# Kernel tuning notes

Hardware: AMD Instinct MI355X
Metric: run time of the kernel (lower is better)

The kernel has to match this reference:

```python
import jax, jax.numpy as jnp
import numpy as np

BN_EPS = 1e-5
B, L, D = 16, 2048, 1024
OS = 64          # attnList[0]
NC = 256         # candidates per sample
CLASS_NUM = 8921
LAB = 1024


def setup_inputs() -> dict:
    key = jax.random.key(0)
    ks = jax.random.split(key, 8)
    scale_a = 1.0 / np.sqrt(D)
    return {
        "X": jax.random.normal(ks[0], (B, L, D), jnp.float32),
        "candidate": jax.random.randint(ks[1], (B, NC), 0, CLASS_NUM, jnp.int64),
        "a_w": jax.random.normal(ks[2], (D, OS), jnp.float32) * scale_a,
        "a_b": jnp.zeros((OS,), jnp.float32),
        "h_w": jax.random.normal(ks[3], (D, LAB), jnp.float32) * scale_a,
        "h_b": jnp.zeros((LAB,), jnp.float32),
        "bn_gamma": jax.random.uniform(ks[4], (LAB,), jnp.float32, 0.5, 1.5),
        "bn_beta": jax.random.normal(ks[5], (LAB,), jnp.float32) * 0.1,
        "bn_mean": jnp.zeros((LAB,), jnp.float32),
        "bn_var": jnp.ones((LAB,), jnp.float32),
        "labDescVec": jax.random.normal(ks[6], (CLASS_NUM, LAB), jnp.float32),
    }


def reference(X, candidate, a_w, a_b, h_w, h_b, bn_gamma, bn_beta, bn_mean, bn_var, labDescVec):
    # --- attention-pooling layer (attnList has one entry) ---
    # alpha: softmax over the sequence dim (dim=1 in torch)
    alpha = jax.nn.softmax(jnp.einsum('bld,do->blo', X, a_w) + a_b, axis=1)  # [B,L,OS]
    Xp = jnp.einsum('blo,bld->bod', alpha, X)                                # [B,OS,D]
    Xp = jnp.einsum('bod,dh->boh', Xp, h_w) + h_b                            # [B,OS,LAB]
    # BatchNorm1d over feature dim (eval mode: running stats)
    Xp = (Xp - bn_mean) * (bn_gamma / jnp.sqrt(bn_var + BN_EPS)) + bn_beta
    Xp = jax.nn.relu(Xp)  # dropout is identity at inference
    # --- candidate attention ---
    batchLabelVec = labDescVec[candidate]                                    # [B,NC,LAB]
    scores = jnp.einsum('boh,bch->boc', Xp, batchLabelVec)                   # [B,OS,NC]
    alpha2 = jax.nn.softmax(scores, axis=1)                                  # softmax over OS (dim=1)
    out = jnp.einsum('boc,boh->bch', alpha2, Xp)                             # [B,NC,LAB]
    return out
```

## Files before the change

kernel.cpp:

```cpp
#include <hip/hip_runtime.h>
#include <hip/hip_bf16.h>
#include <math.h>

#define Bb   16
#define Ll   2048
#define Dd   1024
#define OSo  64
#define NCc  256
#define LABh 1024
#define BN_EPS 1e-5f

typedef short s8v  __attribute__((ext_vector_type(8)));
typedef short s4v  __attribute__((ext_vector_type(4)));
typedef float f32x4 __attribute__((ext_vector_type(4)));

__device__ __forceinline__ short f2b(float f) {
    __hip_bfloat16 h = __float2bfloat16(f);
    short s;
    __builtin_memcpy(&s, &h, 2);
    return s;
}
__device__ __forceinline__ float b2f(short s) {
    union { unsigned u; float f; } v; v.u = ((unsigned)(unsigned short)s) << 16;
    return v.f;
}
__device__ __forceinline__ void g2lds16(const void* g, void* l) {
    __builtin_amdgcn_global_load_lds(
        (const __attribute__((address_space(1))) void*)g,
        (__attribute__((address_space(3))) void*)l, 16, 0, 0);
}
__device__ __forceinline__ void fastbar() {
    asm volatile("s_waitcnt lgkmcnt(0)\n\ts_barrier" ::: "memory");
}
__device__ __forceinline__ int swi(int row, int kElem) {
    return (row * 128 + ((kElem * 2) ^ ((row & 7) << 4))) >> 1;
}
__device__ __forceinline__ f32x4 MF(s8v a, s8v b, f32x4 c) {
    return __builtin_amdgcn_mfma_f32_16x16x32_bf16(a, b, c, 0, 0, 0);
}

__global__ __launch_bounds__(256) void k0(const float* __restrict__ h_w,
                                          const float* __restrict__ a_w,
                                          short* __restrict__ h_wT,
                                          short* __restrict__ a_wT) {
    __shared__ float t[64][68];
    const int tid = threadIdx.x, id = blockIdx.x;
    const float* src; short* dst; int srw, d0, y0;
    if (id < 256) { src = h_w; dst = h_wT; srw = LABh; d0 = (id & 15) * 64; y0 = (id >> 4) * 64; }
    else          { src = a_w; dst = a_wT; srw = OSo;  d0 = (id - 256) * 64; y0 = 0; }
    const int r = tid >> 2, cofs = (tid & 3) * 16;
    #pragma unroll
    for (int w = 0; w < 4; ++w) {
        float4 v = *(const float4*)&src[(size_t)(d0 + r) * srw + y0 + cofs + w * 4];
        t[r][cofs + w * 4 + 0] = v.x;
        t[r][cofs + w * 4 + 1] = v.y;
        t[r][cofs + w * 4 + 2] = v.z;
        t[r][cofs + w * 4 + 3] = v.w;
    }
    __syncthreads();
    s8v o0, o1;
    #pragma unroll
    for (int e = 0; e < 8; ++e) { o0[e] = f2b(t[cofs + e][r]); o1[e] = f2b(t[cofs + 8 + e][r]); }
    *(s8v*)&dst[(size_t)(y0 + r) * Dd + d0 + cofs]     = o0;
    *(s8v*)&dst[(size_t)(y0 + r) * Dd + d0 + cofs + 8] = o1;
}

__global__ __launch_bounds__(256) void k1(const float* __restrict__ X,
                                          const short* __restrict__ a_wT,
                                          float* __restrict__ St) {
    __shared__ __align__(16) char smem[49152];
    float (*ts)[65] = (float(*)[65])smem;
    const int tid = threadIdx.x, lane = tid & 63, wave = tid >> 6;
    const int wm = wave >> 1, wn = wave & 1;
    const int b = blockIdx.y, l0 = blockIdx.x * 64;
    const float* Xb = X + ((size_t)b * Ll + l0) * Dd;
    const int akb = (lane & 15) * 16;
    const int bkb = (lane & 7) * 16;
    f32x4 acc[2][2] = {};

    auto issue = [&](int t, int k0) {
        char* Ab = smem + (t & 1) * 16384;
        #pragma unroll
        for (int q = 0; q < 4; ++q) {
            const int chunk = wave * 4 + q;
            const int row = chunk * 4 + (lane >> 4);
            const char* g = (const char*)Xb + (size_t)row * 4096 + k0 * 4
                          + (akb ^ ((row & 7) << 4));
            g2lds16(g, Ab + chunk * 1024);
        }
        char* Bbuf = smem + 32768 + (t & 1) * 8192;
        #pragma unroll
        for (int q = 0; q < 2; ++q) {
            const int chunk = wave * 2 + q;
            const int row = chunk * 8 + (lane >> 3);
            const char* g = (const char*)a_wT + (size_t)row * 2048 + k0 * 2
                          + (bkb ^ ((row & 7) << 4));
            g2lds16(g, Bbuf + chunk * 1024);
        }
    };

    issue(0, 0);
    #pragma unroll
    for (int t = 0; t < 16; ++t) {
        if (t < 15) issue(t + 1, (t + 1) * 64);
        __syncthreads();
        const char* Ab = smem + (t & 1) * 16384;
        const char* Bbuf = smem + 32768 + (t & 1) * 8192;
        #pragma unroll
        for (int kk = 0; kk < 2; ++kk) {
            s8v a[2], bv[2];
            #pragma unroll
            for (int i = 0; i < 2; ++i) {
                const int row = wm * 32 + i * 16 + (lane & 15);
                const int sw = (row & 7) << 4;
                const int kbyte = kk * 128 + (lane >> 4) * 32;
                float4 v0 = *(const float4*)(Ab + row * 256 + ((kbyte) ^ sw));
                float4 v1 = *(const float4*)(Ab + row * 256 + ((kbyte + 16) ^ sw));
                s8v s;
                s[0]=f2b(v0.x); s[1]=f2b(v0.y); s[2]=f2b(v0.z); s[3]=f2b(v0.w);
                s[4]=f2b(v1.x); s[5]=f2b(v1.y); s[6]=f2b(v1.z); s[7]=f2b(v1.w);
                a[i] = s;
            }
            #pragma unroll
            for (int j = 0; j < 2; ++j) {
                const int row = wn * 32 + j * 16 + (lane & 15);
                const int sw = (row & 7) << 4;
                const int kbyte = kk * 64 + (lane >> 4) * 16;
                bv[j] = *(const s8v*)(Bbuf + row * 128 + (kbyte ^ sw));
            }
            #pragma unroll
            for (int i = 0; i < 2; ++i)
                #pragma unroll
                for (int j = 0; j < 2; ++j)
                    acc[i][j] = MF(a[i], bv[j], acc[i][j]);
        }
        __syncthreads();
    }
    #pragma unroll
    for (int i = 0; i < 2; ++i)
        #pragma unroll
        for (int j = 0; j < 2; ++j)
            #pragma unroll
            for (int rr = 0; rr < 4; ++rr)
                ts[wm * 32 + i * 16 + (lane >> 4) * 4 + rr][wn * 32 + j * 16 + (lane & 15)] = acc[i][j][rr];
    __syncthreads();
    const int o = tid >> 2, lofs = (tid & 3) * 16;
    float* Sp = St + ((size_t)b * OSo + o) * Ll + l0 + lofs;
    #pragma unroll
    for (int w = 0; w < 4; ++w) {
        float4 v;
        v.x = ts[lofs + w * 4 + 0][o];
        v.y = ts[lofs + w * 4 + 1][o];
        v.z = ts[lofs + w * 4 + 2][o];
        v.w = ts[lofs + w * 4 + 3][o];
        *(float4*)&Sp[w * 4] = v;
    }
}

__global__ __launch_bounds__(256) void k2(const float* __restrict__ St,
                                          const float* __restrict__ a_b,
                                          short* __restrict__ aBf) {
    __shared__ float row[Ll];
    __shared__ float red[8];
    const float* p0 = St + (size_t)blockIdx.x * Ll;
    short* ab = aBf + (size_t)blockIdx.x * Ll;
    const int tid = threadIdx.x;
    const int wave = tid >> 6, lane = tid & 63;
    const float bias = a_b[blockIdx.x & (OSo - 1)];
    const int base = tid * 4;
    float m = -1e30f;
    #pragma unroll
    for (int i = base; i < Ll; i += 1024) {
        float4 a = *(const float4*)&p0[i];
        float4 v;
        v.x = a.x + bias; v.y = a.y + bias;
        v.z = a.z + bias; v.w = a.w + bias;
        *(float4*)&row[i] = v;
        m = fmaxf(m, fmaxf(fmaxf(v.x, v.y), fmaxf(v.z, v.w)));
    }
    #pragma unroll
    for (int off = 32; off; off >>= 1) m = fmaxf(m, __shfl_down(m, off));
    if (lane == 0) red[wave] = m;
    __syncthreads();
    if (tid == 0) red[4] = fmaxf(fmaxf(red[0], red[1]), fmaxf(red[2], red[3]));
    __syncthreads();
    const float M = red[4];
    float s = 0.f;
    #pragma unroll
    for (int i = base; i < Ll; i += 1024) {
        float4 v = *(const float4*)&row[i];
        v.x = __expf(v.x - M); v.y = __expf(v.y - M);
        v.z = __expf(v.z - M); v.w = __expf(v.w - M);
        *(float4*)&row[i] = v;
        s += (v.x + v.y) + (v.z + v.w);
    }
    __syncthreads();
    #pragma unroll
    for (int off = 32; off; off >>= 1) s += __shfl_down(s, off);
    if (lane == 0) red[wave] = s;
    __syncthreads();
    if (tid == 0) red[4] = 1.f / (red[0] + red[1] + red[2] + red[3]);
    __syncthreads();
    const float inv = red[4];
    #pragma unroll
    for (int i = base; i < Ll; i += 1024) {
        float4 v = *(const float4*)&row[i];
        s4v o;
        o[0] = f2b(v.x * inv); o[1] = f2b(v.y * inv);
        o[2] = f2b(v.z * inv); o[3] = f2b(v.w * inv);
        *(s4v*)&ab[i] = o;
    }
}

struct R3 { s8v al[2]; float4 xv[4]; };

__global__ __launch_bounds__(256) void k3(const float* __restrict__ X,
                                          const short* __restrict__ aBf,
                                          float* __restrict__ XpP) {
    __shared__ __align__(16) char smem[32768];
    float (*ts)[68] = (float(*)[68])smem;
    const int tid = threadIdx.x;
    const int lane = tid & 63, wave = tid >> 6;
    const int wm = wave >> 1, wn = wave & 1;
    const int id = blockIdx.x;
    const int slot = id >> 3;
    const int b = (id & 7) * 2 + (slot >> 5);
    const int inner = slot & 31;
    const int dt = inner & 15, z = inner >> 4;
    const int d0 = dt * 64;
    const float* Xb = X + (size_t)b * Ll * Dd;
    const short* ab = aBf + (size_t)b * OSo * Ll;
    float* outP = XpP + (size_t)z * ((size_t)Bb * OSo * Dd);
    f32x4 acc[2][2] = {};
    const int arow = tid >> 2, akofs = (tid & 3) * 16;
    const int lq = tid & 15, dq = tid >> 4;
    const int lbase = z * 1024;
    R3 cur, nxt;
    #pragma unroll
    for (int w = 0; w < 2; ++w)
        cur.al[w] = *(const s8v*)&ab[(size_t)arow * Ll + lbase + akofs + w * 8];
    #pragma unroll
    for (int i = 0; i < 4; ++i)
        cur.xv[i] = *(const float4*)&Xb[(size_t)(lbase + lq * 4 + i) * Dd + d0 + dq * 4];
    #pragma unroll
    for (int t = 0; t < 16; ++t) {
        short* Aal = (short*)(smem + (t & 1) * 8192);
        short* Xs  = (short*)(smem + 16384 + (t & 1) * 8192);
        #pragma unroll
        for (int w = 0; w < 2; ++w)
            *(s8v*)&Aal[swi(arow, akofs + w * 8)] = cur.al[w];
        {
            const float* f = (const float*)cur.xv;
            #pragma unroll
            for (int j = 0; j < 4; ++j) {
                const int rowd = dq * 4 + j;
                s4v sj;
                sj[0] = f2b(f[0 * 4 + j]);
                sj[1] = f2b(f[1 * 4 + j]);
                sj[2] = f2b(f[2 * 4 + j]);
                sj[3] = f2b(f[3 * 4 + j]);
                *(s4v*)&Xs[swi(rowd, lq * 4)] = sj;
            }
        }
        fastbar();
        if (t < 15) {
            const int l0 = lbase + (t + 1) * 64;
            #pragma unroll
            for (int w = 0; w < 2; ++w)
                nxt.al[w] = *(const s8v*)&ab[(size_t)arow * Ll + l0 + akofs + w * 8];
            #pragma unroll
            for (int i = 0; i < 4; ++i)
                nxt.xv[i] = *(const float4*)&Xb[(size_t)(l0 + lq * 4 + i) * Dd + d0 + dq * 4];
        }
        #pragma unroll
        for (int kk = 0; kk < 2; ++kk) {
            const int kb = kk * 32 + (lane >> 4) * 8;
            s8v a[2], bb[2];
            #pragma unroll
            for (int i = 0; i < 2; ++i)
                a[i] = *(const s8v*)&Aal[swi(wm * 32 + i * 16 + (lane & 15), kb)];
            #pragma unroll
            for (int j = 0; j < 2; ++j)
                bb[j] = *(const s8v*)&Xs[swi(wn * 32 + j * 16 + (lane & 15), kb)];
            #pragma unroll
            for (int i = 0; i < 2; ++i)
                #pragma unroll
                for (int j = 0; j < 2; ++j)
                    acc[i][j] = MF(a[i], bb[j], acc[i][j]);
        }
        if (t < 15) cur = nxt;
    }
    __syncthreads();
    #pragma unroll
    for (int i = 0; i < 2; ++i)
        #pragma unroll
        for (int j = 0; j < 2; ++j)
            #pragma unroll
            for (int rr = 0; rr < 4; ++rr)
                ts[wm * 32 + i * 16 + (lane >> 4) * 4 + rr][wn * 32 + j * 16 + (lane & 15)] = acc[i][j][rr];
    __syncthreads();
    const int o = tid >> 2, dofs = (tid & 3) * 16;
    float* op = outP + ((size_t)b * OSo + o) * Dd + d0 + dofs;
    #pragma unroll
    for (int w = 0; w < 4; ++w)
        *(float4*)&op[w * 4] = *(float4*)&ts[o][dofs + w * 4];
}

struct R4 { float4 p[8]; s8v w[2]; };

__global__ __launch_bounds__(256) void k4(const float* __restrict__ XpP,
                                          const short* __restrict__ h_wT,
                                          const float* __restrict__ h_b,
                                          const float* __restrict__ gamma,
                                          const float* __restrict__ beta,
                                          const float* __restrict__ mean,
                                          const float* __restrict__ var,
                                          short* __restrict__ Xh) {
    __shared__ __align__(16) char smem[32768];
    short* tsb = (short*)smem;
    const int tid = threadIdx.x, lane = tid & 63, wave = tid >> 6;
    const int wm = wave >> 1, wn = wave & 1;
    const int id = blockIdx.x;
    const int slot = id >> 3;
    const int mt = (id & 7) * 2 + (slot >> 4);
    const int ht = slot & 15;
    const int h0 = ht * 64, m0 = mt * 64;
    const int r = tid >> 2, kofs = (tid & 3) * 16;
    const size_t ZS = (size_t)Bb * OSo * Dd;
    f32x4 acc[2][2] = {};
    R4 cur, nxt;
    #pragma unroll
    for (int w = 0; w < 2; ++w) {
        const float* p0 = XpP + (size_t)(m0 + r) * Dd + kofs + w * 8;
        cur.p[w*4+0] = *(const float4*)&p0[0];
        cur.p[w*4+1] = *(const float4*)&p0[4];
        cur.p[w*4+2] = *(const float4*)&p0[ZS];
        cur.p[w*4+3] = *(const float4*)&p0[ZS + 4];
        cur.w[w]     = *(const s8v*)&h_wT[(size_t)(h0 + r) * Dd + kofs + w * 8];
    }
    #pragma unroll
    for (int t = 0; t < 16; ++t) {
        short* As = (short*)(smem + (t & 1) * 8192);
        short* Bs = (short*)(smem + 16384 + (t & 1) * 8192);
        #pragma unroll
        for (int w = 0; w < 2; ++w) {
            const float* f0 = (const float*)&cur.p[w*4];
            const float* f1 = (const float*)&cur.p[w*4+2];
            s8v s;
            #pragma unroll
            for (int e = 0; e < 8; ++e) s[e] = f2b(f0[e] + f1[e]);
            *(s8v*)&As[swi(r, kofs + w * 8)] = s;
            *(s8v*)&Bs[swi(r, kofs + w * 8)] = cur.w[w];
        }
        fastbar();
        if (t < 15) {
            const int k0 = (t + 1) * 64;
            #pragma unroll
            for (int w = 0; w < 2; ++w) {
                const float* p0 = XpP + (size_t)(m0 + r) * Dd + k0 + kofs + w * 8;
                nxt.p[w*4+0] = *(const float4*)&p0[0];
                nxt.p[w*4+1] = *(const float4*)&p0[4];
                nxt.p[w*4+2] = *(const float4*)&p0[ZS];
                nxt.p[w*4+3] = *(const float4*)&p0[ZS + 4];
                nxt.w[w]     = *(const s8v*)&h_wT[(size_t)(h0 + r) * Dd + k0 + kofs + w * 8];
            }
        }
        #pragma unroll
        for (int kk = 0; kk < 2; ++kk) {
            const int kb = kk * 32 + (lane >> 4) * 8;
            s8v a[2], bb[2];
            #pragma unroll
            for (int i = 0; i < 2; ++i)
                a[i] = *(const s8v*)&As[swi(wm * 32 + i * 16 + (lane & 15), kb)];
            #pragma unroll
            for (int j = 0; j < 2; ++j)
                bb[j] = *(const s8v*)&Bs[swi(wn * 32 + j * 16 + (lane & 15), kb)];
            #pragma unroll
            for (int i = 0; i < 2; ++i)
                #pragma unroll
                for (int j = 0; j < 2; ++j)
                    acc[i][j] = MF(a[i], bb[j], acc[i][j]);
        }
        if (t < 15) cur = nxt;
    }
    __syncthreads();
    #pragma unroll
    for (int j = 0; j < 2; ++j) {
        const int h = h0 + wn * 32 + j * 16 + (lane & 15);
        const float sc = gamma[h] * rsqrtf(var[h] + BN_EPS);
        const float of = (h_b[h] - mean[h]) * sc + beta[h];
        #pragma unroll
        for (int i = 0; i < 2; ++i)
            #pragma unroll
            for (int rr = 0; rr < 4; ++rr) {
                const int ml = wm * 32 + i * 16 + (lane >> 4) * 4 + rr;
                tsb[ml * 64 + wn * 32 + j * 16 + (lane & 15)] = f2b(fmaxf(0.f, acc[i][j][rr] * sc + of));
            }
    }
    __syncthreads();
    #pragma unroll
    for (int w = 0; w < 2; ++w)
        *(s8v*)&Xh[(size_t)(m0 + r) * LABh + h0 + kofs + w * 8] = *(const s8v*)&tsb[r * 64 + kofs + w * 8];
}

struct R56 { float4 ld; s8v xh[2]; };

__global__ __launch_bounds__(256) void k56(const int* __restrict__ cand,
                                           const float* __restrict__ labD,
                                           const short* __restrict__ Xh,
                                           float* __restrict__ out) {
    __shared__ __align__(16) char smem[20608];
    float (*ts)[68] = (float(*)[68])smem;
    float (*al)[64] = (float(*)[64])(smem + 4608);
    int* cidx = (int*)(smem + 20480);
    const int tid = threadIdx.x, lane = tid & 63, wave = tid >> 6;
    const int id = blockIdx.x;
    const int slot = id >> 3;
    const int b = (id & 7) * 2 + (slot >> 4);
    const int c0 = (slot & 15) * 16;
    if (tid < 16) cidx[tid] = cand[b * NCc + c0 + tid];
    __syncthreads();
    const int ar = tid >> 4, ak = (tid & 15) * 4;
    const int br = tid >> 2, bk = (tid & 3) * 16;
    const float* lrow = labD + (size_t)cidx[ar] * LABh;
    const short* xb = Xh + (size_t)b * OSo * LABh;
    f32x4 acc = {};
    R56 cur, nxt;
    cur.ld    = *(const float4*)&lrow[ak];
    cur.xh[0] = *(const s8v*)&xb[(size_t)br * LABh + bk];
    cur.xh[1] = *(const s8v*)&xb[(size_t)br * LABh + bk + 8];
    #pragma unroll
    for (int t = 0; t < 16; ++t) {
        short* As = (short*)(smem + (t & 1) * 10240);
        short* Bs = As + 1024;
        {
            s4v sa;
            sa[0] = f2b(cur.ld.x); sa[1] = f2b(cur.ld.y);
            sa[2] = f2b(cur.ld.z); sa[3] = f2b(cur.ld.w);
            *(s4v*)&As[swi(ar, ak)] = sa;
            *(s8v*)&Bs[swi(br, bk)]     = cur.xh[0];
            *(s8v*)&Bs[swi(br, bk + 8)] = cur.xh[1];
        }
        fastbar();
        if (t < 15) {
            const int k0 = (t + 1) * 64;
            nxt.ld    = *(const float4*)&lrow[k0 + ak];
            nxt.xh[0] = *(const s8v*)&xb[(size_t)br * LABh + k0 + bk];
            nxt.xh[1] = *(const s8v*)&xb[(size_t)br * LABh + k0 + bk + 8];
        }
        #pragma unroll
        for (int kk = 0; kk < 2; ++kk) {
            const int kb = kk * 32 + (lane >> 4) * 8;
            s8v a  = *(const s8v*)&As[swi(lane & 15, kb)];
            s8v bv = *(const s8v*)&Bs[swi(wave * 16 + (lane & 15), kb)];
            acc = MF(a, bv, acc);
        }
        if (t < 15) cur = nxt;
    }
    __syncthreads();
    #pragma unroll
    for (int rr = 0; rr < 4; ++rr)
        ts[(lane >> 4) * 4 + rr][wave * 16 + (lane & 15)] = acc[rr];
    __syncthreads();
    {
        const int cl = tid >> 4, t16 = tid & 15;
        float v[4];
        float m = -1e30f;
        #pragma unroll
        for (int j = 0; j < 4; ++j) { v[j] = ts[cl][t16 + j * 16]; m = fmaxf(m, v[j]); }
        #pragma unroll
        for (int off = 8; off; off >>= 1) m = fmaxf(m, __shfl_xor(m, off, 16));
        float s = 0.f;
        #pragma unroll
        for (int j = 0; j < 4; ++j) { v[j] = __expf(v[j] - m); s += v[j]; }
        #pragma unroll
        for (int off = 8; off; off >>= 1) s += __shfl_xor(s, off, 16);
        const float inv = 1.f / s;
        #pragma unroll
        for (int j = 0; j < 4; ++j) al[cl][t16 + j * 16] = v[j] * inv;
    }
    __syncthreads();
    const int h0 = tid * 4;
    float acc2[16][4] = {};
    for (int o = 0; o < OSo; ++o) {
        s4v xv = *(const s4v*)&xb[(size_t)o * LABh + h0];
        const float x0 = b2f(xv[0]), x1 = b2f(xv[1]), x2 = b2f(xv[2]), x3 = b2f(xv[3]);
        #pragma unroll
        for (int c = 0; c < 16; ++c) {
            const float w = al[c][o];
            acc2[c][0] += w * x0; acc2[c][1] += w * x1;
            acc2[c][2] += w * x2; acc2[c][3] += w * x3;
        }
    }
    #pragma unroll
    for (int c = 0; c < 16; ++c) {
        float4 v; v.x = acc2[c][0]; v.y = acc2[c][1]; v.z = acc2[c][2]; v.w = acc2[c][3];
        *(float4*)&out[((size_t)b * NCc + c0 + c) * LABh + h0] = v;
    }
}

extern "C" void kernel_launch(void* const* d_in, const int* in_sizes, int n_in,
                              void* d_out, int out_size, void* d_ws, size_t ws_size,
                              hipStream_t stream) {
    (void)in_sizes; (void)n_in; (void)out_size; (void)ws_size;
    const float* X      = (const float*)d_in[0];
    const int*   cand   = (const int*)  d_in[1];
    const float* a_w    = (const float*)d_in[2];
    const float* a_b    = (const float*)d_in[3];
    const float* h_w    = (const float*)d_in[4];
    const float* h_b    = (const float*)d_in[5];
    const float* gamma  = (const float*)d_in[6];
    const float* beta   = (const float*)d_in[7];
    const float* mean   = (const float*)d_in[8];
    const float* var    = (const float*)d_in[9];
    const float* labDesc= (const float*)d_in[10];
    float* outp = (float*)d_out;

    char* ws = (char*)d_ws;
    float* St   = (float*)ws;
    float* XpP  = (float*)ws;
    short* aBf  = (short*)(ws + ((size_t)16 << 20));
    short* Xh   = (short*)(ws + ((size_t)20 << 20));
    short* a_wT = (short*)(ws + ((size_t)26 << 20));
    short* h_wT = (short*)(ws + ((size_t)27 << 20));

    k0 <<<272,          256, 0, stream>>>(h_w, a_w, h_wT, a_wT);
    k1 <<<dim3(32, 16), 256, 0, stream>>>(X, a_wT, St);
    k2 <<<Bb * OSo,     256, 0, stream>>>(St, a_b, aBf);
    k3 <<<512,          256, 0, stream>>>(X, aBf, XpP);
    k4 <<<256,          256, 0, stream>>>(XpP, h_wT, h_b, gamma, beta, mean, var, Xh);
    k56<<<256,          256, 0, stream>>>(cand, labDesc, Xh, outp);
}
```

Before: 99.51 us.

## Store attention-pooled partials in bf16 and relax k1 pipeline barriers

k3 now writes its split-L partial sums of the pooled features as bf16 instead of fp32, and k4 reads and adds them as bf16. This halves the intermediate traffic between the two kernels but rounds each partial before summation. In k1 the full __syncthreads is replaced with explicit vmcnt/lgkmcnt waits, so the next tile's async global-to-LDS loads stay in flight while the current tile is computed.

After: 94.48 us (median of 2 runs). -5.1%, faster.

```diff
diff --git a/kernel.cpp b/kernel.cpp
--- a/kernel.cpp
+++ b/kernel.cpp
@@ -31,6 +31,12 @@
 }
 __device__ __forceinline__ void fastbar() {
     asm volatile("s_waitcnt lgkmcnt(0)\n\ts_barrier" ::: "memory");
+}
+__device__ __forceinline__ void dmabar6() {
+    asm volatile("s_waitcnt vmcnt(6) lgkmcnt(0)\n\ts_barrier" ::: "memory");
+}
+__device__ __forceinline__ void dmabar0() {
+    asm volatile("s_waitcnt vmcnt(0) lgkmcnt(0)\n\ts_barrier" ::: "memory");
 }
 __device__ __forceinline__ int swi(int row, int kElem) {
     return (row * 128 + ((kElem * 2) ^ ((row & 7) << 4))) >> 1;
@@ -102,8 +108,8 @@
     issue(0, 0);
     #pragma unroll
     for (int t = 0; t < 16; ++t) {
-        if (t < 15) issue(t + 1, (t + 1) * 64);
-        __syncthreads();
+        if (t < 15) { issue(t + 1, (t + 1) * 64); dmabar6(); }
+        else        { dmabar0(); }
         const char* Ab = smem + (t & 1) * 16384;
         const char* Bbuf = smem + 32768 + (t & 1) * 8192;
         #pragma unroll
@@ -134,8 +140,9 @@
                 for (int j = 0; j < 2; ++j)
                     acc[i][j] = MF(a[i], bv[j], acc[i][j]);
         }
-        __syncthreads();
-    }
+        fastbar();
+    }
+    __syncthreads();
     #pragma unroll
     for (int i = 0; i < 2; ++i)
         #pragma unroll
@@ -216,7 +223,7 @@
 
 __global__ __launch_bounds__(256) void k3(const float* __restrict__ X,
                                           const short* __restrict__ aBf,
-                                          float* __restrict__ XpP) {
+                                          short* __restrict__ XpP) {
     __shared__ __align__(16) char smem[32768];
     float (*ts)[68] = (float(*)[68])smem;
     const int tid = threadIdx.x;
@@ -230,7 +237,7 @@
     const int d0 = dt * 64;
     const float* Xb = X + (size_t)b * Ll * Dd;
     const short* ab = aBf + (size_t)b * OSo * Ll;
-    float* outP = XpP + (size_t)z * ((size_t)Bb * OSo * Dd);
+    short* outP = XpP + (size_t)z * ((size_t)Bb * OSo * Dd);
     f32x4 acc[2][2] = {};
     const int arow = tid >> 2, akofs = (tid & 3) * 16;
     const int lq = tid & 15, dq = tid >> 4;
@@ -300,15 +307,21 @@
                 ts[wm * 32 + i * 16 + (lane >> 4) * 4 + rr][wn * 32 + j * 16 + (lane & 15)] = acc[i][j][rr];
     __syncthreads();
     const int o = tid >> 2, dofs = (tid & 3) * 16;
-    float* op = outP + ((size_t)b * OSo + o) * Dd + d0 + dofs;
-    #pragma unroll
-    for (int w = 0; w < 4; ++w)
-        *(float4*)&op[w * 4] = *(float4*)&ts[o][dofs + w * 4];
-}
-
-struct R4 { float4 p[8]; s8v w[2]; };
-
-__global__ __launch_bounds__(256) void k4(const float* __restrict__ XpP,
+    short* op = outP + ((size_t)b * OSo + o) * Dd + d0 + dofs;
+    #pragma unroll
+    for (int w = 0; w < 2; ++w) {
+        float4 v0 = *(const float4*)&ts[o][dofs + w * 8];
+        float4 v1 = *(const float4*)&ts[o][dofs + w * 8 + 4];
+        s8v s;
+        s[0]=f2b(v0.x); s[1]=f2b(v0.y); s[2]=f2b(v0.z); s[3]=f2b(v0.w);
+        s[4]=f2b(v1.x); s[5]=f2b(v1.y); s[6]=f2b(v1.z); s[7]=f2b(v1.w);
+        *(s8v*)&op[w * 8] = s;
+    }
+}
+
+struct R4 { s8v p[4]; s8v w[2]; };
+
+__global__ __launch_bounds__(256) void k4(const short* __restrict__ XpP,
                                           const short* __restrict__ h_wT,
                                           const float* __restrict__ h_b,
                                           const float* __restrict__ gamma,
@@ -331,11 +344,9 @@
     R4 cur, nxt;
     #pragma unroll
     for (int w = 0; w < 2; ++w) {
-        const float* p0 = XpP + (size_t)(m0 + r) * Dd + kofs + w * 8;
-        cur.p[w*4+0] = *(const float4*)&p0[0];
-        cur.p[w*4+1] = *(const float4*)&p0[4];
-        cur.p[w*4+2] = *(const float4*)&p0[ZS];
-        cur.p[w*4+3] = *(const float4*)&p0[ZS + 4];
+        const short* p0 = XpP + (size_t)(m0 + r) * Dd + kofs + w * 8;
+        cur.p[w*2]   = *(const s8v*)&p0[0];
+        cur.p[w*2+1] = *(const s8v*)&p0[ZS];
         cur.w[w]     = *(const s8v*)&h_wT[(size_t)(h0 + r) * Dd + kofs + w * 8];
     }
     #pragma unroll
@@ -344,11 +355,10 @@
         short* Bs = (short*)(smem + 16384 + (t & 1) * 8192);
         #pragma unroll
         for (int w = 0; w < 2; ++w) {
-            const float* f0 = (const float*)&cur.p[w*4];
-            const float* f1 = (const float*)&cur.p[w*4+2];
+            s8v q0 = cur.p[w*2], q1 = cur.p[w*2+1];
             s8v s;
             #pragma unroll
-            for (int e = 0; e < 8; ++e) s[e] = f2b(f0[e] + f1[e]);
+            for (int e = 0; e < 8; ++e) s[e] = f2b(b2f(q0[e]) + b2f(q1[e]));
             *(s8v*)&As[swi(r, kofs + w * 8)] = s;
             *(s8v*)&Bs[swi(r, kofs + w * 8)] = cur.w[w];
         }
@@ -357,11 +367,9 @@
             const int k0 = (t + 1) * 64;
             #pragma unroll
             for (int w = 0; w < 2; ++w) {
-                const float* p0 = XpP + (size_t)(m0 + r) * Dd + k0 + kofs + w * 8;
-                nxt.p[w*4+0] = *(const float4*)&p0[0];
-                nxt.p[w*4+1] = *(const float4*)&p0[4];
-                nxt.p[w*4+2] = *(const float4*)&p0[ZS];
-                nxt.p[w*4+3] = *(const float4*)&p0[ZS + 4];
+                const short* p0 = XpP + (size_t)(m0 + r) * Dd + k0 + kofs + w * 8;
+                nxt.p[w*2]   = *(const s8v*)&p0[0];
+                nxt.p[w*2+1] = *(const s8v*)&p0[ZS];
                 nxt.w[w]     = *(const s8v*)&h_wT[(size_t)(h0 + r) * Dd + k0 + kofs + w * 8];
             }
         }
@@ -518,7 +526,7 @@
 
     char* ws = (char*)d_ws;
     float* St   = (float*)ws;
-    float* XpP  = (float*)ws;
+    short* XpP  = (short*)ws;
     short* aBf  = (short*)(ws + ((size_t)16 << 20));
     short* Xh   = (short*)(ws + ((size_t)20 << 20));
     short* a_wT = (short*)(ws + ((size_t)26 << 20));
```
